# Kernel optimization log

Measured on AMD Instinct MI355X. Metric: run time of the kernel, lower is better.

Reference implementation:

```python
import jax, jax.numpy as jnp
import numpy as np

N, CIN, H, W = 4, 64, 48, 48
COUT = 64
SCALE, CHUNK, N_HASHES = 2, 144, 4
L = (H * SCALE) * (W * SCALE)                            # 9216 tokens after upsample
HASH_BUCKETS = min(L // CHUNK + (L // CHUNK) % 2, 128)   # 64


def setup_inputs() -> dict:
    key = jax.random.key(0)
    ks = jax.random.split(key, 6)
    cm = COUT // 2
    return {
        "x":   jax.random.normal(ks[0], (N, CIN, H, W), jnp.float32),
        "w1":  jax.random.normal(ks[1], (COUT, CIN, 3, 3), jnp.float32) * 0.05,
        "b1":  jnp.zeros((COUT,), jnp.float32),
        "w2":  jax.random.normal(ks[2], (COUT, COUT, 3, 3), jnp.float32) * 0.05,
        "b2":  jnp.zeros((COUT,), jnp.float32),
        "wm":  jax.random.normal(ks[3], (cm, COUT, 3, 3), jnp.float32) * 0.05,   # conv_match 3x3
        "bm":  jnp.zeros((cm,), jnp.float32),
        "wa":  jax.random.normal(ks[4], (COUT, COUT, 1, 1), jnp.float32) * 0.05, # conv_assembly 1x1
        "ba":  jnp.zeros((COUT,), jnp.float32),
        "rot": jax.random.normal(ks[5], (cm, N_HASHES, HASH_BUCKETS // 2), jnp.float32),  # LSH rotations
    }


def conv2d(x, w, b, pad):
    y = jax.lax.conv_general_dilated(x, w, (1, 1), [(pad, pad), (pad, pad)],
                                     dimension_numbers=("NCHW", "OIHW", "NCHW"))
    return y + b[None, :, None, None]


def _gather(e, i):  # batched index select: e [n,l,c], i [n,m] -> [n,m,c]
    return jax.vmap(lambda a, b: a[b])(e, i)


def _adjacent(x):  # concat each chunk with its circularly previous/next chunk along key dim
    back = jnp.roll(x, 1, axis=2)
    fwd = jnp.roll(x, -1, axis=2)
    return jnp.concatenate([x, back, fwd], axis=3)


def nlsa(x, wm, bm, wa, ba, rot):
    n, co, h, w = x.shape
    l = h * w
    x_embed = conv2d(x, wm, bm, 1).reshape(n, -1, l).transpose(0, 2, 1)  # [n,l,cm]
    y_embed = conv2d(x, wa, ba, 0).reshape(n, -1, l).transpose(0, 2, 1)  # [n,l,co]
    cm = x_embed.shape[-1]
    # --- LSH hashing (argmax over signed random rotations) ---
    rv = jnp.einsum('btf,fhi->bhti', x_embed, rot)       # [n,nh,l,buckets/2]
    rv = jnp.concatenate([rv, -rv], axis=-1)
    codes = jnp.argmax(rv, axis=-1)                      # [n,nh,l]
    codes = codes + (jnp.arange(N_HASHES) * HASH_BUCKETS)[None, :, None]
    codes = codes.reshape(n, -1)                         # [n, nh*l]
    idx = jnp.argsort(codes, axis=-1)
    undo = jnp.argsort(idx, axis=-1)
    mod_idx = idx % l
    # --- sort tokens by bucket, chunk, attend within chunk + adjacent chunks ---
    xs = _gather(x_embed, mod_idx).reshape(n, N_HASHES, l // CHUNK, CHUNK, cm)
    ys = _gather(y_embed, mod_idx).reshape(n, N_HASHES, l // CHUNK, CHUNK, co)
    xm = xs / jnp.maximum(jnp.linalg.norm(xs, axis=-1, keepdims=True), 5e-5)  # F.normalize eps=5e-5
    xm = _adjacent(xm)                                   # [n,nh,K,3*chunk,cm]
    y3 = _adjacent(ys)                                   # [n,nh,K,3*chunk,co]
    raw = jnp.einsum('bhkie,bhkje->bhkij', xs, xm)       # [n,nh,K,chunk,3*chunk]
    bscore = jax.nn.logsumexp(raw, axis=-1, keepdims=True)
    score = jnp.exp(raw - bscore)
    ret = jnp.einsum('bhkij,bhkje->bhkie', score, y3)    # [n,nh,K,chunk,co]
    ret = ret.reshape(n, N_HASHES * l, co)
    bscore = bscore.reshape(n, N_HASHES * l)
    # --- unsort and combine hash rounds with softmax over logsumexp scores ---
    ret = _gather(ret, undo).reshape(n, N_HASHES, l, co)
    bscore = jnp.take_along_axis(bscore, undo, axis=1).reshape(n, N_HASHES, l, 1)
    probs = jax.nn.softmax(bscore, axis=1)
    out = jnp.sum(ret * probs, axis=1)                   # [n,l,co]
    return out.transpose(0, 2, 1).reshape(n, co, h, w) + x  # res_scale=1 residual


def reference(x, w1, b1, w2, b2, wm, bm, wa, ba, rot):
    n, c, h, w = x.shape
    x = jax.image.resize(x, (n, c, h * SCALE, w * SCALE), method="cubic")  # bicubic, half-pixel
    x = jax.nn.relu(conv2d(x, w1, b1, 1))
    x = jax.nn.relu(conv2d(x, w2, b2, 1))
    return nlsa(x, wm, bm, wa, ba, rot)
```

## Files before the change

### kernel.cpp

```cpp
#include <hip/hip_runtime.h>
#include <math.h>

#define NB 4
#define CIN 64
#define CO 64
#define CM 32
#define H0 48
#define W0 48
#define HH 96
#define WW 96
#define LTOK (HH*WW)
#define NH 4
#define NBUCK 64
#define CHUNK 144
#define NCHUNK 64
#define TOT (NH*LTOK)
#define SB 512
#define NSB (TOT/SB)

typedef __attribute__((ext_vector_type(8))) short short8;
typedef __attribute__((ext_vector_type(4))) short short4v;
typedef __attribute__((ext_vector_type(4))) float f32x4;

__device__ __forceinline__ short f2bf(float f) {
  union { float f; unsigned u; } v; v.f = f;
  unsigned r = v.u + 0x7fffu + ((v.u >> 16) & 1u);
  return (short)(r >> 16);
}
__device__ __forceinline__ short f2bf_fast(float f) {
  union { float f; unsigned u; } v; v.f = f;
  return (short)((v.u + 0x8000u) >> 16);
}
__device__ __forceinline__ float bf2f(short h) {
  union { float f; unsigned u; } v; v.u = ((unsigned)(unsigned short)h) << 16;
  return v.f;
}
__device__ __forceinline__ short8 ld_b64x2(const short* p) {
  short4v a = *(const short4v*)p;
  short4v b = *(const short4v*)(p+4);
  short8 r; r[0]=a[0];r[1]=a[1];r[2]=a[2];r[3]=a[3];r[4]=b[0];r[5]=b[1];r[6]=b[2];r[7]=b[3];
  return r;
}

__device__ __forceinline__ void cubic_taps(int o, int insz, int* p, float* w) {
  int j = o >> 1;
  const float B0=-0.0234375f, B1=0.2265625f, B2=0.8671875f, B3=-0.0703125f;
  if ((o & 1) == 0) { p[0]=j-2;p[1]=j-1;p[2]=j;  p[3]=j+1; w[0]=B0;w[1]=B1;w[2]=B2;w[3]=B3; }
  else              { p[0]=j-1;p[1]=j;  p[2]=j+1;p[3]=j+2; w[0]=B3;w[1]=B2;w[2]=B1;w[3]=B0; }
  float s = 0.f;
  #pragma unroll
  for (int a=0;a<4;a++){ if (p[a] < 0 || p[a] >= insz) p[a] = -1; else s += w[a]; }
  float inv = 1.f / s;
  #pragma unroll
  for (int a=0;a<4;a++) w[a] *= inv;
}

__global__ void k_upsample(const float* __restrict__ x, float* __restrict__ up) {
  int i = blockIdx.x*blockDim.x + threadIdx.x;
  if (i >= NB*CIN*HH*WW) return;
  int ox = i % WW; int t = i / WW;
  int oy = t % HH; t /= HH;
  int c = t % CIN; int n = t / CIN;
  int px[4]; float wx[4]; cubic_taps(ox, W0, px, wx);
  int py[4]; float wy[4]; cubic_taps(oy, H0, py, wy);
  const float* src = x + ((size_t)(n*CIN + c))*H0*W0;
  float acc = 0.f;
  #pragma unroll
  for (int a=0;a<4;a++) {
    if (py[a] < 0) continue;
    const float* r = src + py[a]*W0;
    float ra = 0.f;
    #pragma unroll
    for (int b=0;b<4;b++) if (px[b] >= 0) ra = fmaf(wx[b], r[px[b]], ra);
    acc = fmaf(wy[a], ra, acc);
  }
  up[i] = acc;
}

__global__ void k_wprep3(const float* __restrict__ w1, const float* __restrict__ w2,
                         const float* __restrict__ wm, const float* __restrict__ wa,
                         short* __restrict__ base) {
  int i = blockIdx.x*blockDim.x + threadIdx.x;
  if (i >= 96256) return;
  if (i >= 92160) {
    int j = i - 92160;
    float v = wa[j];
    short hi = f2bf(v);
    base[184320 + j] = hi;
    base[188416 + j] = f2bf(v - bf2f(hi));
    return;
  }
  const float* src; short *dH, *dL; int couts, j;
  if (i < 36864)      { src = w1; couts = 64; j = i;          dH = base;          dL = base + 36864; }
  else if (i < 73728) { src = w2; couts = 64; j = i - 36864;  dH = base + 73728;  dL = base + 110592; }
  else                { src = wm; couts = 32; j = i - 73728;  dH = base + 147456; dL = base + 165888; }
  int ci = j & 63; int t = j >> 6; int co = t % couts; int s = t / couts;
  float v = src[((size_t)(co*64 + ci))*9 + s];
  short hi = f2bf(v);
  dH[j] = hi;
  dL[j] = f2bf(v - bf2f(hi));
}

#define XP 68
#define WP 72
template<int TOKS, bool TMAJ, bool RELU>
__global__ __launch_bounds__(256) void k_conv3m(const float* __restrict__ in,
                          const short* __restrict__ wH, const short* __restrict__ wL,
                          const float* __restrict__ bias, float* __restrict__ out,
                          int couts_tot, int cosplit) {
  int blk = blockIdx.x;
  int ch = blk % cosplit;
  int tb = (blk / cosplit) % (LTOK/TOKS);
  int n  = blk / (cosplit * (LTOK/TOKS));
  int t0 = tb * TOKS;
  int co0 = ch * 32;
  int tid = threadIdx.x;
  int wv = tid >> 6, lane = tid & 63, quad = lane >> 4, l16 = lane & 15;
  __shared__ __align__(16) short XB[TOKS*XP];
  __shared__ __align__(16) short WHs[32*WP];
  __shared__ __align__(16) short WLs[32*WP];
  __shared__ float biasl[32];
  if (tid < 32) biasl[tid] = bias[co0 + tid];
  constexpr int TSH = (TOKS == 128) ? 7 : 6;
  f32x4 acc[2][2];
  #pragma unroll
  for (int a=0;a<2;a++)
    #pragma unroll
    for (int b=0;b<2;b++) acc[a][b] = (f32x4){0.f,0.f,0.f,0.f};

  const float* inb = in + (size_t)n*CIN*LTOK;
  for (int s = 0; s < 9; s++) {
    int dy = s/3 - 1, dx = s%3 - 1;
    __syncthreads();
    #pragma unroll
    for (int it = 0; it < (TOKS*32)/256; it++) {
      int idx = tid + 256*it;
      int tok = idx & (TOKS-1), c = idx >> TSH;
      int t = t0 + tok;
      int y = t / WW, x = t - y*WW;
      int ys = y + dy, xs = x + dx;
      float v0 = 0.f, v1 = 0.f;
      if ((unsigned)ys < HH && (unsigned)xs < WW) {
        const float* p = inb + ((size_t)(2*c))*LTOK + ys*WW + xs;
        v0 = p[0]; v1 = p[LTOK];
      }
      unsigned pk = (unsigned)(unsigned short)f2bf(v0) | (((unsigned)(unsigned short)f2bf(v1)) << 16);
      ((unsigned*)XB)[tok*(XP/2) + c] = pk;
    }
    #pragma unroll
    for (int it = 0; it < 8; it++) {
      int idx = tid + 256*it;
      int plane = idx >> 10, rem = idx & 1023;
      int co = rem >> 5, d = rem & 31;
      const unsigned* srcw = (const unsigned*)(plane ? wL : wH);
      unsigned v = srcw[(size_t)(s*couts_tot + co0 + co)*32 + d];
      unsigned* dst = (unsigned*)(plane ? WLs : WHs);
      dst[co*(WP/2) + d] = v;
    }
    __syncthreads();
    #pragma unroll
    for (int kf = 0; kf < 2; kf++) {
      if (!TMAJ) {
        short8 xf[2];
        #pragma unroll
        for (int nt=0;nt<2;nt++)
          xf[nt] = ld_b64x2(&XB[(wv*32 + nt*16 + l16)*XP + kf*32 + quad*8]);
        #pragma unroll
        for (int mt=0;mt<2;mt++) {
          short8 wh = *(const short8*)&WHs[(mt*16 + l16)*WP + kf*32 + quad*8];
          short8 wl = *(const short8*)&WLs[(mt*16 + l16)*WP + kf*32 + quad*8];
          #pragma unroll
          for (int nt=0;nt<2;nt++) {
            acc[mt][nt] = __builtin_amdgcn_mfma_f32_16x16x32_bf16(wh, xf[nt], acc[mt][nt], 0, 0, 0);
            acc[mt][nt] = __builtin_amdgcn_mfma_f32_16x16x32_bf16(wl, xf[nt], acc[mt][nt], 0, 0, 0);
          }
        }
      } else {
        short8 xf = ld_b64x2(&XB[(wv*16 + l16)*XP + kf*32 + quad*8]);
        #pragma unroll
        for (int nt=0;nt<2;nt++) {
          short8 wh = *(const short8*)&WHs[(nt*16 + l16)*WP + kf*32 + quad*8];
          short8 wl = *(const short8*)&WLs[(nt*16 + l16)*WP + kf*32 + quad*8];
          acc[0][nt] = __builtin_amdgcn_mfma_f32_16x16x32_bf16(xf, wh, acc[0][nt], 0, 0, 0);
          acc[0][nt] = __builtin_amdgcn_mfma_f32_16x16x32_bf16(xf, wl, acc[0][nt], 0, 0, 0);
        }
      }
    }
  }
  if (!TMAJ) {
    #pragma unroll
    for (int mt=0;mt<2;mt++) {
      #pragma unroll
      for (int nt=0;nt<2;nt++) {
        int tokl = wv*32 + nt*16 + l16;
        #pragma unroll
        for (int reg=0;reg<4;reg++) {
          int col = mt*16 + quad*4 + reg;
          float v = acc[mt][nt][reg] + biasl[col];
          if (RELU) v = fmaxf(v, 0.f);
          out[((size_t)(n*couts_tot + co0 + col))*LTOK + t0 + tokl] = v;
        }
      }
    }
  } else {
    #pragma unroll
    for (int nt=0;nt<2;nt++) {
      int co = nt*16 + l16;
      #pragma unroll
      for (int reg=0;reg<4;reg++) {
        int t = t0 + wv*16 + quad*4 + reg;
        float v = acc[0][nt][reg] + biasl[co];
        if (RELU) v = fmaxf(v, 0.f);
        out[((size_t)n*LTOK + t)*couts_tot + co] = v;
      }
    }
  }
}

__global__ __launch_bounds__(256) void k_conv1x1m(const float* __restrict__ in,
                          const short* __restrict__ wH, const short* __restrict__ wL,
                          const float* __restrict__ bias, short* __restrict__ out) {
  int blk = blockIdx.x;
  int n  = blk / 144;
  int t0 = (blk % 144) * 64;
  int tid = threadIdx.x;
  int wv = tid >> 6, lane = tid & 63, quad = lane >> 4, l16 = lane & 15;
  __shared__ __align__(16) short XB[64*XP];
  __shared__ __align__(16) short WHs[64*WP];
  __shared__ __align__(16) short WLs[64*WP];
  __shared__ float biasl[64];
  if (tid < 64) biasl[tid] = bias[tid];
  const float* inb = in + (size_t)n*CIN*LTOK;
  #pragma unroll
  for (int it = 0; it < 8; it++) {
    int idx = tid + 256*it;
    int tok = idx & 63, c = idx >> 6;
    const float* p = inb + ((size_t)(2*c))*LTOK + t0 + tok;
    float v0 = p[0], v1 = p[LTOK];
    unsigned pk = (unsigned)(unsigned short)f2bf(v0) | (((unsigned)(unsigned short)f2bf(v1)) << 16);
    ((unsigned*)XB)[tok*(XP/2) + c] = pk;
  }
  #pragma unroll
  for (int it = 0; it < 16; it++) {
    int idx = tid + 256*it;
    int plane = idx >> 11, rem = idx & 2047;
    int co = rem >> 5, d = rem & 31;
    const unsigned* srcw = (const unsigned*)(plane ? wL : wH);
    unsigned v = srcw[(size_t)co*32 + d];
    unsigned* dst = (unsigned*)(plane ? WLs : WHs);
    dst[co*(WP/2) + d] = v;
  }
  __syncthreads();
  f32x4 acc[4];
  #pragma unroll
  for (int i=0;i<4;i++) acc[i] = (f32x4){0.f,0.f,0.f,0.f};
  #pragma unroll
  for (int kf = 0; kf < 2; kf++) {
    short8 xf = ld_b64x2(&XB[(wv*16 + l16)*XP + kf*32 + quad*8]);
    #pragma unroll
    for (int nt=0;nt<4;nt++) {
      short8 wh = *(const short8*)&WHs[(nt*16 + l16)*WP + kf*32 + quad*8];
      short8 wl = *(const short8*)&WLs[(nt*16 + l16)*WP + kf*32 + quad*8];
      acc[nt] = __builtin_amdgcn_mfma_f32_16x16x32_bf16(xf, wh, acc[nt], 0, 0, 0);
      acc[nt] = __builtin_amdgcn_mfma_f32_16x16x32_bf16(xf, wl, acc[nt], 0, 0, 0);
    }
  }
  #pragma unroll
  for (int nt=0;nt<4;nt++) {
    int co = nt*16 + l16;
    #pragma unroll
    for (int reg=0;reg<4;reg++) {
      int t = t0 + wv*16 + quad*4 + reg;
      out[((size_t)n*LTOK + t)*CO + co] = f2bf(acc[nt][reg] + biasl[co]);
    }
  }
}

__global__ void k_hash(const float* __restrict__ xe, const float* __restrict__ rot,
                       int* __restrict__ codes, int* __restrict__ hist,
                       short* __restrict__ xqb, short* __restrict__ xkb,
                       float* __restrict__ qnb) {
  int b  = blockIdx.x;
  int n  = b / NSB;
  int bb = b % NSB;
  int j  = bb*SB + threadIdx.x;
  int h  = j / LTOK;
  int t  = j % LTOK;
  __shared__ float rl[CM][NBUCK/2];
  __shared__ int lh[256];
  for (int e = threadIdx.x; e < 256; e += SB) lh[e] = 0;
  for (int e = threadIdx.x; e < CM*(NBUCK/2); e += SB) {
    int f = e / 32, i = e % 32;
    rl[f][i] = rot[(f*NH + h)*32 + i];
  }
  __syncthreads();
  float q[CM];
  const float4* xr4 = (const float4*)(xe + ((size_t)n*LTOK + t)*CM);
  #pragma unroll
  for (int r = 0; r < 8; r++) {
    float4 v = xr4[r];
    q[4*r+0]=v.x; q[4*r+1]=v.y; q[4*r+2]=v.z; q[4*r+3]=v.w;
  }
  if (bb < LTOK/SB) {
    float ssq = 0.f;
    #pragma unroll
    for (int f = 0; f < CM; f++) ssq = fmaf(q[f], q[f], ssq);
    float nrm = sqrtf(ssq);
    float rn = 1.f / fmaxf(nrm, 5e-5f);
    qnb[(size_t)n*LTOK + t] = nrm;
    #pragma unroll
    for (int r = 0; r < 4; r++) {
      short8 q8, k8;
      #pragma unroll
      for (int jj = 0; jj < 8; jj++) { q8[jj] = f2bf(q[8*r+jj]); k8[jj] = f2bf(q[8*r+jj]*rn); }
      *(short8*)&xqb[((size_t)n*LTOK + t)*CM + 8*r] = q8;
      *(short8*)&xkb[((size_t)n*LTOK + t)*CM + 8*r] = k8;
    }
  }
  float bp = -INFINITY, bn = -INFINITY; int ip = 0, inn = 0;
  for (int i = 0; i < 32; i++) {
    float acc = 0.f;
    #pragma unroll
    for (int f = 0; f < CM; f++) acc = fmaf(q[f], rl[f][i], acc);
    if (acc  > bp) { bp = acc;  ip  = i; }
    if (-acc > bn) { bn = -acc; inn = i; }
  }
  int code = (bp >= bn) ? ip : (32 + inn);
  code += h * NBUCK;
  codes[n*TOT + j] = code;
  atomicAdd(&lh[code], 1);
  __syncthreads();
  for (int e = threadIdx.x; e < 256; e += SB) hist[((size_t)(n*256 + e))*NSB + bb] = lh[e];
}

__global__ void k_offsets(const int* __restrict__ hist, int* __restrict__ bstart) {
  int n = blockIdx.x; int c = threadIdx.x;
  const int* hrow = hist + (size_t)(n*256 + c)*NSB;
  int tot = 0;
  for (int b = 0; b < NSB; b++) tot += hrow[b];
  __shared__ int sc[256];
  sc[c] = tot;
  __syncthreads();
  for (int d = 1; d < 256; d <<= 1) {
    int u = (c >= d) ? sc[c-d] : 0;
    __syncthreads();
    sc[c] += u;
    __syncthreads();
  }
  int run = sc[c] - tot;
  int* brow = bstart + (size_t)(n*256 + c)*NSB;
  for (int b = 0; b < NSB; b++) {
    brow[b] = run;
    run += hrow[b];
  }
}

__global__ void k_scatter(const int* __restrict__ codes, const int* __restrict__ bstart,
                          int* __restrict__ sidx) {
  int b = blockIdx.x; int n = b / NSB; int bb = b % NSB;
  int tid = threadIdx.x;
  int j = bb*SB + tid;
  int code = codes[n*TOT + j];
  int wave = tid >> 6, lane = tid & 63;
  __shared__ int wcnt[8][256];
  for (int e = tid; e < 8*256; e += SB) ((int*)wcnt)[e] = 0;
  __syncthreads();
  unsigned long long mask = ~0ULL;
  #pragma unroll
  for (int bit = 0; bit < 8; bit++) {
    unsigned long long bal = __ballot((code >> bit) & 1);
    mask &= ((code >> bit) & 1) ? bal : ~bal;
  }
  unsigned long long lt = (lane == 63) ? 0x7FFFFFFFFFFFFFFFULL : ((1ULL << lane) - 1ULL);
  int rank_w = __popcll(mask & lt);
  if (rank_w == 0) wcnt[wave][code] = __popcll(mask);
  __syncthreads();
  int rank = rank_w;
  for (int w2 = 0; w2 < 8; w2++) {
    if (w2 >= wave) break;
    rank += wcnt[w2][code];
  }
  int pos = bstart[((size_t)(n*256 + code))*NSB + bb] + rank;
  sidx[n*TOT + pos] = j;
}

#define PQP 168
__global__ __launch_bounds__(192,1) void k_attn(const short* __restrict__ xqb,
                       const short* __restrict__ xkb, const float* __restrict__ qnb,
                       const short* __restrict__ yvb, const int* __restrict__ sidx,
                       short* __restrict__ ret, float* __restrict__ bsc) {
  int raw = blockIdx.x;
  int xcd = raw & 7;
  int n = xcd >> 1;
  int idx2 = ((raw >> 3) << 1) | (xcd & 1);
  int h = idx2 >> 5;
  int cpair = idx2 & 31;
  const int base = n*TOT + h*LTOK;
  __shared__ __align__(16) short Pq[144*PQP];
  __shared__ __align__(16) short VbT[64*PQP];
  __shared__ int sj[3*CHUNK];
  int tid = threadIdx.x;
  int w = tid >> 6, lane = tid & 63, quad = lane >> 4, l16 = lane & 15;
  const short* xq = xqb + (size_t)n*LTOK*CM;
  const short* xk = xkb + (size_t)n*LTOK*CM;
  const short* yv = yvb + (size_t)n*LTOK*CO;
  const float* qn = qnb + (size_t)n*LTOK;

  for (int e = tid; e < 144*8; e += 192) {
    int r = e >> 3, d = e & 7;
    ((unsigned*)Pq)[r*(PQP/2) + 72 + d] = 0u;
  }
  for (int e = tid; e < 64*8; e += 192) {
    int r = e >> 3, d = e & 7;
    ((unsigned*)VbT)[r*(PQP/2) + 72 + d] = 0u;
  }

  for (int ch2 = 0; ch2 < 2; ch2++) {
    int kch = cpair*2 + ch2;
    int kprev = (kch + NCHUNK - 1) & (NCHUNK-1), knext = (kch + 1) & (NCHUNK-1);
    __syncthreads();
    for (int e = tid; e < 3*CHUNK; e += 192) {
      int tt = e / CHUNK, r = e - tt*CHUNK;
      int kk = (tt==0) ? kch : ((tt==1) ? kprev : knext);
      sj[e] = sidx[base + kk*CHUNK + r];
    }
    __syncthreads();
    short8 qfrag[3]; float m_ln[3][4];
    #pragma unroll
    for (int mt=0;mt<3;mt++) {
      int tok = sj[48*w + 16*mt + l16] % LTOK;
      qfrag[mt] = *(const short8*)(xq + (size_t)tok*CM + quad*8);
      #pragma unroll
      for (int r=0;r<4;r++)
        m_ln[mt][r] = qn[sj[48*w + 16*mt + 4*quad + r] % LTOK];
    }
    f32x4 acc[3][4];
    #pragma unroll
    for (int mt=0;mt<3;mt++)
      #pragma unroll
      for (int nt=0;nt<4;nt++) acc[mt][nt] = (f32x4){0.f,0.f,0.f,0.f};
    float sspart[12];
    #pragma unroll
    for (int i=0;i<12;i++) sspart[i]=0.f;

    for (int tt = 0; tt < 3; tt++) {
      __syncthreads();
      #pragma unroll
      for (int it = 0; it < 6; it++) {
        int idx = tid + 192*it;
        int g = idx / CHUNK, key = idx - g*CHUNK;
        int tok = sj[tt*CHUNK + key] % LTOK;
        short8 v = *(const short8*)(yv + (size_t)tok*CO + 8*g);
        #pragma unroll
        for (int i=0;i<8;i++) VbT[(8*g+i)*PQP + key] = v[i];
      }
      __syncthreads();
      int ktok[9];
      #pragma unroll
      for (int nt=0;nt<9;nt++) ktok[nt] = sj[tt*CHUNK + 16*nt + l16] % LTOK;
      #pragma unroll
      for (int nt = 0; nt < 9; nt++) {
        short8 bfr = *(const short8*)(xk + (size_t)ktok[nt]*CM + quad*8);
        f32x4 c[3];
        #pragma unroll
        for (int mt=0;mt<3;mt++)
          c[mt] = __builtin_amdgcn_mfma_f32_16x16x32_bf16(qfrag[mt], bfr, (f32x4){0.f,0.f,0.f,0.f}, 0, 0, 0);
        #pragma unroll
        for (int mt=0;mt<3;mt++) {
          #pragma unroll
          for (int reg=0;reg<4;reg++) {
            float p = __expf(c[mt][reg] - m_ln[mt][reg]);
            sspart[mt*4+reg] += p;
            Pq[(48*w + 16*mt + 4*quad + reg)*PQP + 16*nt + l16] = f2bf_fast(p);
          }
        }
      }
      #pragma unroll
      for (int kf = 0; kf < 5; kf++) {
        short8 afr[3];
        #pragma unroll
        for (int mt=0;mt<3;mt++)
          afr[mt] = *(const short8*)&Pq[(48*w + 16*mt + l16)*PQP + kf*32 + quad*8];
        #pragma unroll
        for (int nt2=0;nt2<4;nt2++) {
          short8 vfr = *(const short8*)&VbT[(16*nt2 + l16)*PQP + kf*32 + quad*8];
          #pragma unroll
          for (int mt=0;mt<3;mt++)
            acc[mt][nt2] = __builtin_amdgcn_mfma_f32_16x16x32_bf16(afr[mt], vfr, acc[mt][nt2], 0, 0, 0);
        }
      }
    }
    #pragma unroll
    for (int i=0;i<12;i++) {
      float v = sspart[i];
      v += __shfl_xor(v, 1); v += __shfl_xor(v, 2);
      v += __shfl_xor(v, 4); v += __shfl_xor(v, 8);
      sspart[i] = v;
    }
    #pragma unroll
    for (int mt=0;mt<3;mt++) {
      #pragma unroll
      for (int reg=0;reg<4;reg++) {
        int row = 48*w + 16*mt + 4*quad + reg;
        int mtok = sj[row];
        float ssum = sspart[mt*4+reg];
        float inv = 1.f / ssum;
        short* rp = ret + ((size_t)n*TOT + mtok)*CO;
        #pragma unroll
        for (int nt2=0;nt2<4;nt2++) rp[16*nt2 + l16] = f2bf(acc[mt][nt2][reg] * inv);
        if (l16 == 0) bsc[(size_t)n*TOT + mtok] = m_ln[mt][reg] + logf(ssum);
      }
    }
  }
}

__global__ void k_combine(const short* __restrict__ ret, const float* __restrict__ bsc,
                          const float* __restrict__ c2, float* __restrict__ out) {
  int blk = blockIdx.x;
  int n  = blk / (LTOK/16);
  int t0 = (blk % (LTOK/16)) * 16;
  __shared__ float rl[NH][16][CO+1];
  __shared__ float pw[NH][16];
  int tid = threadIdx.x;
  for (int h = 0; h < NH; h++)
    for (int e = tid; e < 16*CO; e += 256) {
      int tl = e >> 6, f = e & 63;
      rl[h][tl][f] = bf2f(ret[((size_t)n*TOT + h*LTOK + t0 + tl)*CO + f]);
    }
  if (tid < 16) {
    float b0[NH]; float mm = -INFINITY;
    #pragma unroll
    for (int h = 0; h < NH; h++) { b0[h] = bsc[(size_t)n*TOT + h*LTOK + t0 + tid]; mm = fmaxf(mm, b0[h]); }
    float s = 0.f;
    #pragma unroll
    for (int h = 0; h < NH; h++) { b0[h] = __expf(b0[h] - mm); s += b0[h]; }
    float inv = 1.f / s;
    #pragma unroll
    for (int h = 0; h < NH; h++) pw[h][tid] = b0[h] * inv;
  }
  __syncthreads();
  int tl = tid & 15;
  int cog = tid >> 4;
  #pragma unroll
  for (int cc = 0; cc < 4; cc++) {
    int co = cog + 16*cc;
    size_t oi = ((size_t)(n*CO + co))*LTOK + t0 + tl;
    float a = c2[oi];
    #pragma unroll
    for (int h = 0; h < NH; h++) a = fmaf(pw[h][tl], rl[h][tl][co], a);
    out[oi] = a;
  }
}

extern "C" void kernel_launch(void* const* d_in, const int* in_sizes, int n_in,
                              void* d_out, int out_size, void* d_ws, size_t ws_size,
                              hipStream_t stream) {
  const float* x   = (const float*)d_in[0];
  const float* w1  = (const float*)d_in[1];
  const float* b1  = (const float*)d_in[2];
  const float* w2  = (const float*)d_in[3];
  const float* b2  = (const float*)d_in[4];
  const float* wm  = (const float*)d_in[5];
  const float* bm  = (const float*)d_in[6];
  const float* wa  = (const float*)d_in[7];
  const float* ba  = (const float*)d_in[8];
  const float* rot = (const float*)d_in[9];
  float* out = (float*)d_out;

  float* ws  = (float*)d_ws;
  float* up  = ws;
  float* c1  = up  + 2359296;
  float* c2  = c1  + 2359296;
  float* xep = c2  + 2359296;
  float* bsc = xep + 1179648;
  short* ret = (short*)(bsc + 147456);
  int* codes  = (int*)(ret + 9437184);
  int* sidx   = codes + 147456;
  int* hist   = sidx + 147456;
  int* bstart = hist + 73728;
  short* wpk = (short*)(bstart + 73728);
  short* w1H = wpk;
  short* w1L = wpk + 36864;
  short* w2H = wpk + 73728;
  short* w2L = wpk + 110592;
  short* wmH = wpk + 147456;
  short* wmL = wpk + 165888;
  short* waH = wpk + 184320;
  short* waL = wpk + 188416;
  short* xqb = (short*)up;
  short* xkb = xqb + 1179648;
  float* qnb = (float*)(xkb + 1179648);
  short* yvb = (short*)c1;
  (void)in_sizes; (void)n_in; (void)out_size; (void)ws_size;

  k_wprep3<<<dim3((96256 + 255)/256), dim3(256), 0, stream>>>(w1, w2, wm, wa, wpk);
  k_upsample<<<dim3((NB*CIN*HH*WW + 255)/256), dim3(256), 0, stream>>>(x, up);
  k_conv3m<128,false,true><<<dim3(NB*72*2), dim3(256), 0, stream>>>(up, w1H, w1L, b1, c1, 64, 2);
  k_conv3m<128,false,true><<<dim3(NB*72*2), dim3(256), 0, stream>>>(c1, w2H, w2L, b2, c2, 64, 2);
  k_conv3m<64,true,false><<<dim3(NB*144), dim3(256), 0, stream>>>(c2, wmH, wmL, bm, xep, 32, 1);
  k_conv1x1m<<<dim3(NB*144), dim3(256), 0, stream>>>(c2, waH, waL, ba, yvb);
  k_hash<<<dim3(NB*NSB), dim3(SB), 0, stream>>>(xep, rot, codes, hist, xqb, xkb, qnb);
  k_offsets<<<dim3(NB), dim3(256), 0, stream>>>(hist, bstart);
  k_scatter<<<dim3(NB*NSB), dim3(SB), 0, stream>>>(codes, bstart, sidx);
  k_attn<<<dim3(NB*NH*NCHUNK/2), dim3(192), 0, stream>>>(xqb, xkb, qnb, yvb, sidx, ret, bsc);
  k_combine<<<dim3(NB*(LTOK/16)), dim3(256), 0, stream>>>(ret, bsc, c2, out);
}
```

Before: 350.8 us.

## Store intermediate activations as packed bf16 channel pairs and shrink conv tiles

```diff
diff --git a/kernel.cpp b/kernel.cpp
--- a/kernel.cpp
+++ b/kernel.cpp
@@ -27,6 +27,9 @@
   unsigned r = v.u + 0x7fffu + ((v.u >> 16) & 1u);
   return (short)(r >> 16);
 }
+__device__ __forceinline__ unsigned packbf(float a, float b) {
+  return (unsigned)(unsigned short)f2bf(a) | (((unsigned)(unsigned short)f2bf(b)) << 16);
+}
 __device__ __forceinline__ short f2bf_fast(float f) {
   union { float f; unsigned u; } v; v.f = f;
   return (short)((v.u + 0x8000u) >> 16);
@@ -55,26 +58,31 @@
   for (int a=0;a<4;a++) w[a] *= inv;
 }
 
-__global__ void k_upsample(const float* __restrict__ x, float* __restrict__ up) {
+__global__ void k_upsample(const float* __restrict__ x, unsigned* __restrict__ upb) {
   int i = blockIdx.x*blockDim.x + threadIdx.x;
-  if (i >= NB*CIN*HH*WW) return;
+  if (i >= NB*32*HH*WW) return;
   int ox = i % WW; int t = i / WW;
   int oy = t % HH; t /= HH;
-  int c = t % CIN; int n = t / CIN;
+  int c2 = t % 32; int n = t / 32;
   int px[4]; float wx[4]; cubic_taps(ox, W0, px, wx);
   int py[4]; float wy[4]; cubic_taps(oy, H0, py, wy);
-  const float* src = x + ((size_t)(n*CIN + c))*H0*W0;
-  float acc = 0.f;
-  #pragma unroll
-  for (int a=0;a<4;a++) {
-    if (py[a] < 0) continue;
-    const float* r = src + py[a]*W0;
-    float ra = 0.f;
-    #pragma unroll
-    for (int b=0;b<4;b++) if (px[b] >= 0) ra = fmaf(wx[b], r[px[b]], ra);
-    acc = fmaf(wy[a], ra, acc);
-  }
-  up[i] = acc;
+  float a01[2];
+  #pragma unroll
+  for (int cc = 0; cc < 2; cc++) {
+    const float* src = x + ((size_t)(n*CIN + 2*c2 + cc))*H0*W0;
+    float acc = 0.f;
+    #pragma unroll
+    for (int a=0;a<4;a++) {
+      if (py[a] < 0) continue;
+      const float* r = src + py[a]*W0;
+      float ra = 0.f;
+      #pragma unroll
+      for (int b=0;b<4;b++) if (px[b] >= 0) ra = fmaf(wx[b], r[px[b]], ra);
+      acc = fmaf(wy[a], ra, acc);
+    }
+    a01[cc] = acc;
+  }
+  upb[((size_t)(n*32 + c2))*LTOK + oy*WW + ox] = packbf(a01[0], a01[1]);
 }
 
 __global__ void k_wprep3(const float* __restrict__ w1, const float* __restrict__ w2,
@@ -103,48 +111,41 @@
 
 #define XP 68
 #define WP 72
-template<int TOKS, bool TMAJ, bool RELU>
-__global__ __launch_bounds__(256) void k_conv3m(const float* __restrict__ in,
+template<bool TMAJ, bool RELU, bool WF, bool WB>
+__global__ __launch_bounds__(256) void k_conv3m(const unsigned* __restrict__ in,
                           const short* __restrict__ wH, const short* __restrict__ wL,
-                          const float* __restrict__ bias, float* __restrict__ out,
-                          int couts_tot, int cosplit) {
+                          const float* __restrict__ bias, float* __restrict__ outF,
+                          unsigned* __restrict__ outB, int couts_tot, int cosplit) {
   int blk = blockIdx.x;
   int ch = blk % cosplit;
-  int tb = (blk / cosplit) % (LTOK/TOKS);
-  int n  = blk / (cosplit * (LTOK/TOKS));
-  int t0 = tb * TOKS;
+  int tb = (blk / cosplit) % 144;
+  int n  = blk / (cosplit * 144);
+  int t0 = tb * 64;
   int co0 = ch * 32;
   int tid = threadIdx.x;
   int wv = tid >> 6, lane = tid & 63, quad = lane >> 4, l16 = lane & 15;
-  __shared__ __align__(16) short XB[TOKS*XP];
+  __shared__ __align__(16) short XB[64*XP];
   __shared__ __align__(16) short WHs[32*WP];
   __shared__ __align__(16) short WLs[32*WP];
   __shared__ float biasl[32];
   if (tid < 32) biasl[tid] = bias[co0 + tid];
-  constexpr int TSH = (TOKS == 128) ? 7 : 6;
-  f32x4 acc[2][2];
-  #pragma unroll
-  for (int a=0;a<2;a++)
-    #pragma unroll
-    for (int b=0;b<2;b++) acc[a][b] = (f32x4){0.f,0.f,0.f,0.f};
-
-  const float* inb = in + (size_t)n*CIN*LTOK;
+  f32x4 acc[2];
+  acc[0] = (f32x4){0.f,0.f,0.f,0.f}; acc[1] = (f32x4){0.f,0.f,0.f,0.f};
+
+  const unsigned* inb = in + (size_t)n*32*LTOK;
   for (int s = 0; s < 9; s++) {
     int dy = s/3 - 1, dx = s%3 - 1;
     __syncthreads();
     #pragma unroll
-    for (int it = 0; it < (TOKS*32)/256; it++) {
+    for (int it = 0; it < 8; it++) {
       int idx = tid + 256*it;
-      int tok = idx & (TOKS-1), c = idx >> TSH;
+      int tok = idx & 63, c = idx >> 6;
       int t = t0 + tok;
       int y = t / WW, x = t - y*WW;
       int ys = y + dy, xs = x + dx;
-      float v0 = 0.f, v1 = 0.f;
-      if ((unsigned)ys < HH && (unsigned)xs < WW) {
-        const float* p = inb + ((size_t)(2*c))*LTOK + ys*WW + xs;
-        v0 = p[0]; v1 = p[LTOK];
-      }
-      unsigned pk = (unsigned)(unsigned short)f2bf(v0) | (((unsigned)(unsigned short)f2bf(v1)) << 16);
+      unsigned pk = 0;
+      if ((unsigned)ys < HH && (unsigned)xs < WW)
+        pk = inb[(size_t)c*LTOK + ys*WW + xs];
       ((unsigned*)XB)[tok*(XP/2) + c] = pk;
     }
     #pragma unroll
@@ -160,46 +161,47 @@
     __syncthreads();
     #pragma unroll
     for (int kf = 0; kf < 2; kf++) {
+      short8 xf = ld_b64x2(&XB[(wv*16 + l16)*XP + kf*32 + quad*8]);
       if (!TMAJ) {
-        short8 xf[2];
-        #pragma unroll
-        for (int nt=0;nt<2;nt++)
-          xf[nt] = ld_b64x2(&XB[(wv*32 + nt*16 + l16)*XP + kf*32 + quad*8]);
         #pragma unroll
         for (int mt=0;mt<2;mt++) {
           short8 wh = *(const short8*)&WHs[(mt*16 + l16)*WP + kf*32 + quad*8];
           short8 wl = *(const short8*)&WLs[(mt*16 + l16)*WP + kf*32 + quad*8];
-          #pragma unroll
-          for (int nt=0;nt<2;nt++) {
-            acc[mt][nt] = __builtin_amdgcn_mfma_f32_16x16x32_bf16(wh, xf[nt], acc[mt][nt], 0, 0, 0);
-            acc[mt][nt] = __builtin_amdgcn_mfma_f32_16x16x32_bf16(wl, xf[nt], acc[mt][nt], 0, 0, 0);
-          }
+          acc[mt] = __builtin_amdgcn_mfma_f32_16x16x32_bf16(wh, xf, acc[mt], 0, 0, 0);
+          acc[mt] = __builtin_amdgcn_mfma_f32_16x16x32_bf16(wl, xf, acc[mt], 0, 0, 0);
         }
       } else {
-        short8 xf = ld_b64x2(&XB[(wv*16 + l16)*XP + kf*32 + quad*8]);
         #pragma unroll
         for (int nt=0;nt<2;nt++) {
           short8 wh = *(const short8*)&WHs[(nt*16 + l16)*WP + kf*32 + quad*8];
           short8 wl = *(const short8*)&WLs[(nt*16 + l16)*WP + kf*32 + quad*8];
-          acc[0][nt] = __builtin_amdgcn_mfma_f32_16x16x32_bf16(xf, wh, acc[0][nt], 0, 0, 0);
-          acc[0][nt] = __builtin_amdgcn_mfma_f32_16x16x32_bf16(xf, wl, acc[0][nt], 0, 0, 0);
+          acc[nt] = __builtin_amdgcn_mfma_f32_16x16x32_bf16(xf, wh, acc[nt], 0, 0, 0);
+          acc[nt] = __builtin_amdgcn_mfma_f32_16x16x32_bf16(xf, wl, acc[nt], 0, 0, 0);
         }
       }
     }
   }
   if (!TMAJ) {
+    int tokl = wv*16 + l16;
     #pragma unroll
     for (int mt=0;mt<2;mt++) {
-      #pragma unroll
-      for (int nt=0;nt<2;nt++) {
-        int tokl = wv*32 + nt*16 + l16;
-        #pragma unroll
-        for (int reg=0;reg<4;reg++) {
-          int col = mt*16 + quad*4 + reg;
-          float v = acc[mt][nt][reg] + biasl[col];
-          if (RELU) v = fmaxf(v, 0.f);
-          out[((size_t)(n*couts_tot + co0 + col))*LTOK + t0 + tokl] = v;
-        }
+      float v[4];
+      #pragma unroll
+      for (int reg=0;reg<4;reg++) {
+        int col = mt*16 + quad*4 + reg;
+        v[reg] = acc[mt][reg] + biasl[col];
+        if (RELU) v[reg] = fmaxf(v[reg], 0.f);
+      }
+      int colb = mt*16 + quad*4;
+      if (WF) {
+        #pragma unroll
+        for (int reg=0;reg<4;reg++)
+          outF[((size_t)(n*couts_tot + co0 + colb + reg))*LTOK + t0 + tokl] = v[reg];
+      }
+      if (WB) {
+        size_t nb = (size_t)n*(couts_tot >> 1);
+        outB[(nb + ((co0 + colb) >> 1))*LTOK + t0 + tokl]     = packbf(v[0], v[1]);
+        outB[(nb + ((co0 + colb + 2) >> 1))*LTOK + t0 + tokl] = packbf(v[2], v[3]);
       }
     }
   } else {
@@ -209,15 +211,15 @@
       #pragma unroll
       for (int reg=0;reg<4;reg++) {
         int t = t0 + wv*16 + quad*4 + reg;
-        float v = acc[0][nt][reg] + biasl[co];
+        float v = acc[nt][reg] + biasl[co];
         if (RELU) v = fmaxf(v, 0.f);
-        out[((size_t)n*LTOK + t)*couts_tot + co] = v;
-      }
-    }
-  }
-}
-
-__global__ __launch_bounds__(256) void k_conv1x1m(const float* __restrict__ in,
+        outF[((size_t)n*LTOK + t)*couts_tot + co] = v;
+      }
+    }
+  }
+}
+
+__global__ __launch_bounds__(256) void k_conv1x1m(const unsigned* __restrict__ in,
                           const short* __restrict__ wH, const short* __restrict__ wL,
                           const float* __restrict__ bias, short* __restrict__ out) {
   int blk = blockIdx.x;
@@ -230,15 +232,12 @@
   __shared__ __align__(16) short WLs[64*WP];
   __shared__ float biasl[64];
   if (tid < 64) biasl[tid] = bias[tid];
-  const float* inb = in + (size_t)n*CIN*LTOK;
+  const unsigned* inb = in + (size_t)n*32*LTOK;
   #pragma unroll
   for (int it = 0; it < 8; it++) {
     int idx = tid + 256*it;
     int tok = idx & 63, c = idx >> 6;
-    const float* p = inb + ((size_t)(2*c))*LTOK + t0 + tok;
-    float v0 = p[0], v1 = p[LTOK];
-    unsigned pk = (unsigned)(unsigned short)f2bf(v0) | (((unsigned)(unsigned short)f2bf(v1)) << 16);
-    ((unsigned*)XB)[tok*(XP/2) + c] = pk;
+    ((unsigned*)XB)[tok*(XP/2) + c] = inb[(size_t)c*LTOK + t0 + tok];
   }
   #pragma unroll
   for (int it = 0; it < 16; it++) {
@@ -587,6 +586,9 @@
   short* wmL = wpk + 165888;
   short* waH = wpk + 184320;
   short* waL = wpk + 188416;
+  unsigned* upb = (unsigned*)up;
+  unsigned* c1b = (unsigned*)c1;
+  unsigned* c2b = (unsigned*)c1 + 1179648;
   short* xqb = (short*)up;
   short* xkb = xqb + 1179648;
   float* qnb = (float*)(xkb + 1179648);
@@ -594,11 +596,11 @@
   (void)in_sizes; (void)n_in; (void)out_size; (void)ws_size;
 
   k_wprep3<<<dim3((96256 + 255)/256), dim3(256), 0, stream>>>(w1, w2, wm, wa, wpk);
-  k_upsample<<<dim3((NB*CIN*HH*WW + 255)/256), dim3(256), 0, stream>>>(x, up);
-  k_conv3m<128,false,true><<<dim3(NB*72*2), dim3(256), 0, stream>>>(up, w1H, w1L, b1, c1, 64, 2);
-  k_conv3m<128,false,true><<<dim3(NB*72*2), dim3(256), 0, stream>>>(c1, w2H, w2L, b2, c2, 64, 2);
-  k_conv3m<64,true,false><<<dim3(NB*144), dim3(256), 0, stream>>>(c2, wmH, wmL, bm, xep, 32, 1);
-  k_conv1x1m<<<dim3(NB*144), dim3(256), 0, stream>>>(c2, waH, waL, ba, yvb);
+  k_upsample<<<dim3((NB*32*HH*WW + 255)/256), dim3(256), 0, stream>>>(x, upb);
+  k_conv3m<false,true,false,true><<<dim3(NB*144*2), dim3(256), 0, stream>>>(upb, w1H, w1L, b1, nullptr, c1b, 64, 2);
+  k_conv3m<false,true,true,true><<<dim3(NB*144*2), dim3(256), 0, stream>>>(c1b, w2H, w2L, b2, c2, c2b, 64, 2);
+  k_conv3m<true,false,true,false><<<dim3(NB*144), dim3(256), 0, stream>>>(c2b, wmH, wmL, bm, xep, nullptr, 32, 1);
+  k_conv1x1m<<<dim3(NB*144), dim3(256), 0, stream>>>(c2b, waH, waL, ba, yvb);
   k_hash<<<dim3(NB*NSB), dim3(SB), 0, stream>>>(xep, rot, codes, hist, xqb, xkb, qnb);
   k_offsets<<<dim3(NB), dim3(256), 0, stream>>>(hist, bstart);
   k_scatter<<<dim3(NB*NSB), dim3(SB), 0, stream>>>(codes, bstart, sidx);
```

Measured after the change: 299.5 us. -14.6%, faster.
